# Kernel tuning notes

Measured on AMD Instinct MI355X. Metric: run time of the kernel, lower is better.

## Reference

```python
import jax, jax.numpy as jnp
import numpy as np

B, T, C, E, H = 4, 2048, 1024, 8, 4096

def setup_inputs() -> dict:
    key = jax.random.key(0)
    ks = jax.random.split(key, 5)
    x = jax.random.normal(ks[0], (B, T, C), dtype=jnp.float32)
    weights = jax.random.uniform(ks[1], (B, T, 2), dtype=jnp.float32)
    gamma = jnp.ones((C,), dtype=jnp.float32)
    beta = jnp.zeros((C,), dtype=jnp.float32)
    W1 = jax.random.normal(ks[2], (E, C, H), dtype=jnp.float32) * 0.02
    W2 = jax.random.normal(ks[3], (E, H, C), dtype=jnp.float32) * 0.02
    winners = jax.random.randint(ks[4], (B, T, 2), 0, E, dtype=jnp.int32)
    return {"x": x, "weights": weights, "gamma": gamma, "beta": beta,
            "W1": W1, "W2": W2, "winners": winners}

def _layernorm(x, gamma, beta, eps=1e-5):
    mu = jnp.mean(x, axis=-1, keepdims=True)
    var = jnp.var(x, axis=-1, keepdims=True)
    return (x - mu) * jax.lax.rsqrt(var + eps) * gamma + beta

def reference(x, weights, gamma, beta, W1, W2, winners):
    # h = ln2(x); then top-2 MoE dispatch/combine as in CaMoE_Block
    h = _layernorm(x, gamma, beta)          # [B,T,C]
    n_experts = W1.shape[0]
    final_out = jnp.zeros_like(h)
    for e in range(n_experts):
        # per-token combine coefficient: sum over the 2 ranks where winner==e
        coef = jnp.sum(jnp.where(winners == e, weights, 0.0), axis=-1)  # [B,T]
        # RWKV channel-mix FFN: relu(h W1)^2 W2
        hidden = jnp.square(jax.nn.relu(jnp.einsum('btc,ch->bth', h, W1[e])))
        expert_out = jnp.einsum('bth,hc->btc', hidden, W2[e])
        final_out = final_out + coef[..., None] * expert_out
    return x + final_out
```

## Files before the change

### kernel.cpp

```cpp
#include <hip/hip_runtime.h>
#include <stddef.h>

typedef unsigned short u16;
typedef unsigned int u32;

#define B_ 4
#define T_ 2048
#define C_ 1024
#define E_ 8
#define H_ 4096
#define NTOK (B_ * T_)
#define NPAIR (NTOK * 2)
#define BM 128
#define BN 128
#define BK 64
#define KSPLIT 2
#define MAXTILES 136
#define MAXROWS (MAXTILES * 128)
#define NWG1 ((H_ / BN) * MAXTILES)

#define NB_C2 2048
#define NB_CP 1024

#define NB_C1 2048
#define NB_LN NTOK
#define NB_CNT (NPAIR / 256)
#define NB_TID (MAXROWS / 1024)
#define NB_TOTAL (NB_C1 + NB_LN + NB_CNT + NB_TID)

typedef __bf16 bf16x8 __attribute__((ext_vector_type(8)));
typedef float f32x4 __attribute__((ext_vector_type(4)));
typedef u16 u16x8 __attribute__((ext_vector_type(8)));

__device__ __forceinline__ u16 f2bf(float f) {
    union { float f; u32 u; } c;
    c.f = f;
    u32 r = c.u + 0x7FFFu + ((c.u >> 16) & 1u);
    return (u16)(r >> 16);
}

__device__ __forceinline__ u32 pk2bf(float a, float b) {
    union { __bf16 h; u16 u; } x, y;
    x.h = (__bf16)a;
    y.h = (__bf16)b;
    return (u32)x.u | ((u32)y.u << 16);
}

__device__ __forceinline__ void gld16(const void* g, void* l) {
    __builtin_amdgcn_global_load_lds(
        (const __attribute__((address_space(1))) u32*)g,
        (__attribute__((address_space(3))) u32*)l, 16, 0, 0);
}


__device__ __forceinline__ void ln_body(
    const float* __restrict__ x, const float* __restrict__ gamma,
    const float* __restrict__ beta, u16* __restrict__ h, int token,
    float* smf) {
    const int t = threadIdx.x;
    const float* xr = x + (size_t)token * C_;
    float4 v = *(const float4*)(xr + t * 4);
    float s = v.x + v.y + v.z + v.w;
    float ss = v.x * v.x + v.y * v.y + v.z * v.z + v.w * v.w;
    #pragma unroll
    for (int off = 32; off > 0; off >>= 1) {
        s += __shfl_down(s, off);
        ss += __shfl_down(ss, off);
    }
    float* ws_s = smf;
    float* ws_q = smf + 4;
    const int wave = t >> 6, lane = t & 63;
    if (lane == 0) { ws_s[wave] = s; ws_q[wave] = ss; }
    __syncthreads();
    float S = ws_s[0] + ws_s[1] + ws_s[2] + ws_s[3];
    float Q = ws_q[0] + ws_q[1] + ws_q[2] + ws_q[3];
    float mu = S * (1.0f / C_);
    float var = Q * (1.0f / C_) - mu * mu;
    float rstd = rsqrtf(var + 1e-5f);
    float4 g = *(const float4*)(gamma + t * 4);
    float4 b = *(const float4*)(beta + t * 4);
    ushort4 hv;
    hv.x = f2bf((v.x - mu) * rstd * g.x + b.x);
    hv.y = f2bf((v.y - mu) * rstd * g.y + b.y);
    hv.z = f2bf((v.z - mu) * rstd * g.z + b.z);
    hv.w = f2bf((v.w - mu) * rstd * g.w + b.w);
    *(ushort4*)(h + (size_t)token * C_ + t * 4) = hv;
}

template <bool PERM>
__device__ __forceinline__ void conv_body(
    const float* __restrict__ in, u16* __restrict__ outp, int K, int N,
    int bid, u16* sm) {
    const int nbx = N >> 8;
    const int nby = K >> 6;
    const int bx = bid % nbx;
    const int by = (bid / nbx) % nby;
    const int e = bid / (nbx * nby);
    const int k0 = by * 64, n0 = bx * 256;
    const int t = threadIdx.x;
    const float* src = in + (size_t)e * K * N;
    u16* dst = outp + (size_t)e * N * K;
    const int cw = t & 63;
    const int rw = t >> 6;
    #pragma unroll
    for (int p = 0; p < 16; ++p) {
        const int r = p * 4 + rw;
        const int kr = PERM ? (((r & 3) << 4) | (r >> 2)) : r;
        float4 v = *(const float4*)(src + (size_t)(k0 + kr) * N + n0 + cw * 4);
        const int base = r * 258 + cw * 4;
        *(u32*)&sm[base + 0] = pk2bf(v.x, v.y);
        *(u32*)&sm[base + 2] = pk2bf(v.z, v.w);
    }
    __syncthreads();
    const u32* smw = (const u32*)sm;
    const int c = t & 7;
    const int ro = t >> 3;
    #pragma unroll
    for (int p = 0; p < 4; ++p) {
        const int np = p * 32 + ro;
        u16x8 lo, hi;
        #pragma unroll
        for (int m = 0; m < 8; ++m) {
            u32 wv = smw[(c * 8 + m) * 129 + np];
            lo[m] = (u16)(wv & 0xFFFFu);
            hi[m] = (u16)(wv >> 16);
        }
        *(u16x8*)(dst + (size_t)(n0 + 2 * np) * K + k0 + c * 8) = lo;
        *(u16x8*)(dst + (size_t)(n0 + 2 * np + 1) * K + k0 + c * 8) = hi;
    }
}

__device__ __forceinline__ void count_body(
    const int* __restrict__ winners, int* __restrict__ counts, int b, int* lc) {
    if (threadIdx.x < E_) lc[threadIdx.x] = 0;
    __syncthreads();
    atomicAdd(&lc[winners[b * 256 + threadIdx.x]], 1);
    __syncthreads();
    if (threadIdx.x < E_) {
        int c = lc[threadIdx.x];
        if (c) atomicAdd(&counts[threadIdx.x], c);
    }
}

__device__ __forceinline__ void copy_body(
    const float* __restrict__ x, float* __restrict__ out, int b) {
    const int t = threadIdx.x;
    const float4* src = (const float4*)x + (size_t)b * 2048;
    float4* dst = (float4*)out + (size_t)b * 2048;
    #pragma unroll
    for (int i = 0; i < 8; ++i) dst[i * 256 + t] = src[i * 256 + t];
}

__global__ __launch_bounds__(256) void fused_pre(
    const float* __restrict__ x, const float* __restrict__ gamma,
    const float* __restrict__ beta, u16* __restrict__ h,
    const int* __restrict__ winners, int* __restrict__ counts,
    const float* __restrict__ W1, u16* __restrict__ W1T,
    int* __restrict__ token_id) {
    __shared__ u16 sm[64 * 258];
    int b = blockIdx.x;
    if (b < NB_C1) { conv_body<false>(W1, W1T, C_, H_, b, sm); return; }
    b -= NB_C1;
    if (b < NB_LN) { ln_body(x, gamma, beta, h, b, (float*)sm); return; }
    b -= NB_LN;
    if (b < NB_CNT) { count_body(winners, counts, b, (int*)sm); return; }
    b -= NB_CNT;
    const int p = (b * 256 + threadIdx.x) * 4;
    if (p < MAXROWS) *(int4*)(token_id + p) = make_int4(-1, -1, -1, -1);
}

__global__ __launch_bounds__(256) void place_kernel(
    const int* __restrict__ winners, const float* __restrict__ wts,
    const int* __restrict__ counts, int* __restrict__ pos,
    int* __restrict__ token_id, float* __restrict__ pair_w,
    int* __restrict__ tile_expert) {
    __shared__ int po[E_ + 1];
    __shared__ int lcount[E_], lbase[E_];
    const int t = threadIdx.x;
    if (t < E_) lcount[t] = 0;
    if (t == 0) {
        int off = 0;
        po[0] = 0;
        #pragma unroll
        for (int e = 0; e < E_; ++e) {
            off += ((counts[e] + 127) >> 7) << 7;
            po[e + 1] = off;
        }
    }
    __syncthreads();
    if (blockIdx.x == 0 && t < MAXTILES) {
        int r = t * 128;
        int ee = -1;
        if (r < po[E_]) {
            ee = 0;
            while (r >= po[ee + 1]) ++ee;
        }
        tile_expert[t] = ee;
    }
    const int p = blockIdx.x * 256 + t;
    const int e = winners[p];
    const int rank = atomicAdd(&lcount[e], 1);
    __syncthreads();
    if (t < E_) {
        int c = lcount[t];
        lbase[t] = c ? atomicAdd(&pos[t], c) : 0;
    }
    __syncthreads();
    const int slot = po[e] + lbase[e] + rank;
    token_id[slot] = p >> 1;
    pair_w[slot] = wts[p];
}

template <bool PHASE2>
__device__ __forceinline__ void gemm_body(
    const u16* __restrict__ Amat, const u16* __restrict__ Bmat,
    const int* __restrict__ token_id, const float* __restrict__ pair_w,
    const int* __restrict__ tile_expert, u16* __restrict__ hidden,
    float* __restrict__ out, const u16* __restrict__ zeropage,
    int bid0, int zi, u16* __restrict__ As, u16* __restrict__ Bs) {
    constexpr int Kdim = PHASE2 ? H_ : C_;
    constexpr int KRANGE = PHASE2 ? (H_ / KSPLIT) : C_;
    constexpr int NWGX = PHASE2 ? (C_ / BN) : (H_ / BN);
    constexpr int NWG = NWGX * MAXTILES;

    int bid = (bid0 & 7) * (NWG >> 3) + (bid0 >> 3);
    const int ct = bid % NWGX;
    const int rt = bid / NWGX;

    const int e = tile_expert[rt];
    if (e < 0) return;
    const int tid = threadIdx.x;
    const int w = tid >> 6;
    const int lane = tid & 63;
    const int n0 = ct * BN;
    const int kbase = PHASE2 ? zi * KRANGE : 0;
    const u16* Bb = Bmat + (size_t)e * H_ * C_;

    const int sub = lane >> 3;
    const size_t koffB = (size_t)(((lane & 7) ^ sub) * 16);

    const char* abase[4];
    bool aval[4];
    const char* bbase[4];
    u16* adst[4];
    u16* bdst[4];
    #pragma unroll
    for (int j = 0; j < 4; ++j) {
        const int lrow32 = w * 32 + j * 8 + sub;
        const int grow = rt * BM + lrow32;
        if (PHASE2) {
            aval[j] = true;
            abase[j] = (const char*)(Amat + (size_t)grow * Kdim + kbase) + koffB;
        } else {
            int tok = token_id[grow];
            aval[j] = tok >= 0;
            abase[j] = (const char*)(Amat + (size_t)(tok < 0 ? 0 : tok) * Kdim) + koffB;
        }
        bbase[j] = (const char*)(Bb + (size_t)(n0 + lrow32) * Kdim + kbase) + koffB;
        adst[j] = &As[(w * 32 + j * 8) * BK];
        bdst[j] = &Bs[(w * 32 + j * 8) * BK];
    }

    const int wr = w >> 1, wc = w & 1;
    const int lrow = lane & 15;
    const int quad = lane >> 4;
    const int rsw = lrow & 7;

    f32x4 acc[4][4] = {};

    for (int k0 = 0; k0 < KRANGE; k0 += BK) {
        __syncthreads();
        const size_t kb = (size_t)k0 * 2;
        #pragma unroll
        for (int j = 0; j < 4; ++j)
            gld16(aval[j] ? abase[j] + kb : (const char*)zeropage, adst[j]);
        #pragma unroll
        for (int j = 0; j < 4; ++j)
            gld16(bbase[j] + kb, bdst[j]);
        __syncthreads();
        #pragma unroll
        for (int kk = 0; kk < 2; ++kk) {
            bf16x8 af[4], bfv[4];
            #pragma unroll
            for (int mi = 0; mi < 4; ++mi) {
                int row = wr * 64 + mi * 16 + lrow;
                int pch = (kk * 4 + quad) ^ rsw;
                af[mi] = *(const bf16x8*)&As[row * BK + pch * 8];
            }
            #pragma unroll
            for (int ni = 0; ni < 4; ++ni) {
                int row = wc * 64 + ni * 16 + lrow;
                int pch = (kk * 4 + quad) ^ rsw;
                bfv[ni] = *(const bf16x8*)&Bs[row * BK + pch * 8];
            }
            #pragma unroll
            for (int mi = 0; mi < 4; ++mi)
                #pragma unroll
                for (int ni = 0; ni < 4; ++ni)
                    acc[mi][ni] = __builtin_amdgcn_mfma_f32_16x16x32_bf16(
                        af[mi], bfv[ni], acc[mi][ni], 0, 0, 0);
        }
    }

    if (!PHASE2) {
        #pragma unroll
        for (int mi = 0; mi < 4; ++mi) {
            int rbase = rt * BM + wr * 64 + mi * 16 + quad * 4;
            #pragma unroll
            for (int j = 0; j < 4; ++j) {
                ushort4 o;
                float v0 = fmaxf(acc[mi][0][j], 0.0f);
                float v1 = fmaxf(acc[mi][1][j], 0.0f);
                float v2 = fmaxf(acc[mi][2][j], 0.0f);
                float v3 = fmaxf(acc[mi][3][j], 0.0f);
                o.x = f2bf(v0 * v0);
                o.y = f2bf(v1 * v1);
                o.z = f2bf(v2 * v2);
                o.w = f2bf(v3 * v3);
                *(ushort4*)&hidden[(size_t)(rbase + j) * H_ + n0 + wc * 64 + lrow * 4] = o;
            }
        }
    } else {
        #pragma unroll
        for (int mi = 0; mi < 4; ++mi) {
            int rbase = rt * BM + wr * 64 + mi * 16 + quad * 4;
            #pragma unroll
            for (int j = 0; j < 4; ++j) {
                int grow = rbase + j;
                int tok = token_id[grow];
                if (tok < 0) continue;
                float pw = pair_w[grow];
                #pragma unroll
                for (int ni = 0; ni < 4; ++ni) {
                    int col = n0 + wc * 64 + ni * 16 + lrow;
                    atomicAdd(&out[(size_t)tok * C_ + col], pw * acc[mi][ni][j]);
                }
            }
        }
    }
}

__global__ __launch_bounds__(256, 4) void gemm1_conv(
    const u16* __restrict__ h, const u16* __restrict__ W1T,
    const int* __restrict__ token_id, const float* __restrict__ pair_w,
    const int* __restrict__ tile_expert, u16* __restrict__ hidden,
    const u16* __restrict__ zeropage, const float* __restrict__ W2,
    u16* __restrict__ W2T, const float* __restrict__ x,
    float* __restrict__ out) {
    __shared__ u16 smu[64 * 258];
    const int b = blockIdx.x;
    if (b < NWG1) {
        gemm_body<false>(h, W1T, token_id, pair_w, tile_expert, hidden,
                         nullptr, zeropage, b, 0, smu, smu + BM * BK);
    } else if (b < NWG1 + NB_C2) {
        conv_body<true>(W2, W2T, H_, C_, b - NWG1, smu);
    } else {
        copy_body(x, out, b - NWG1 - NB_C2);
    }
}

__global__ __launch_bounds__(256, 4) void gemm2_kernel(
    const u16* __restrict__ hidden, const u16* __restrict__ W2T,
    const int* __restrict__ token_id, const float* __restrict__ pair_w,
    const int* __restrict__ tile_expert, float* __restrict__ out,
    const u16* __restrict__ zeropage) {
    __shared__ u16 As[BM * BK];
    __shared__ u16 Bs[BN * BK];
    const int bid = blockIdx.y * (C_ / BN) + blockIdx.x;
    gemm_body<true>(hidden, W2T, token_id, pair_w, tile_expert, nullptr, out,
                    zeropage, bid, blockIdx.z, As, Bs);
}

extern "C" void kernel_launch(void* const* d_in, const int* in_sizes, int n_in,
                              void* d_out, int out_size, void* d_ws, size_t ws_size,
                              hipStream_t stream) {
    const float* x = (const float*)d_in[0];
    const float* weights = (const float*)d_in[1];
    const float* gamma = (const float*)d_in[2];
    const float* beta = (const float*)d_in[3];
    const float* W1 = (const float*)d_in[4];
    const float* W2 = (const float*)d_in[5];
    const int* winners = (const int*)d_in[6];
    float* out = (float*)d_out;

    char* ws = (char*)d_ws;
    const size_t SZ_H = (size_t)NTOK * C_ * 2;
    const size_t SZ_HID = (size_t)MAXROWS * H_ * 2;
    const size_t SZ_WT = (size_t)E_ * H_ * C_ * 2;
    const size_t OFF_HID = SZ_H;
    const size_t OFF_W1T = OFF_HID + SZ_HID;
    const size_t OFF_W2T = OFF_W1T + SZ_WT;
    const size_t OFF_META = OFF_W2T + SZ_WT;

    u16* h = (u16*)ws;
    u16* hidden = (u16*)(ws + OFF_HID);
    u16* W1T = (u16*)(ws + OFF_W1T);
    u16* W2T = (u16*)(ws + OFF_W2T);
    int* meta = (int*)(ws + OFF_META);
    int* counts = meta;
    int* pos = meta + 8;
    u16* zeropage = (u16*)(meta + 32);
    int* tile_expert = meta + 48;
    int* token_id = meta + 192;
    float* pair_w = (float*)(meta + 192 + MAXROWS);

    hipMemsetAsync(meta, 0, 192 * sizeof(int), stream);

    fused_pre<<<NB_TOTAL, 256, 0, stream>>>(x, gamma, beta, h, winners,
                                            counts, W1, W1T, token_id);
    place_kernel<<<NPAIR / 256, 256, 0, stream>>>(winners, weights, counts, pos,
                                                  token_id, pair_w, tile_expert);
    gemm1_conv<<<NWG1 + NB_C2 + NB_CP, 256, 0, stream>>>(
        h, W1T, token_id, pair_w, tile_expert, hidden, zeropage, W2, W2T, x, out);
    gemm2_kernel<<<dim3(C_ / BN, MAXTILES, KSPLIT), 256, 0, stream>>>(
        hidden, W2T, token_id, pair_w, tile_expert, out, zeropage);
}
```

Measured before the change: 696.4 us.

## Merge preprocessing and placement kernels into one persistent kernel with grid barrier

Replaces the fused_pre and place_kernel launches with a single persistent pre_kernel of 512 blocks. Blocks first do counting, token_id init and LayerNorm, then meet at a software grid barrier before placement and W1 transpose-conversion. This removes one kernel launch and its boundary, and lets the W1 conversion run after the barrier. The cost is spin-wait barrier overhead and the risk of deadlock if not all 512 blocks are co-resident.

Result: slower. 740.3 us (+6.3%).

```diff
diff --git a/kernel.cpp b/kernel.cpp
--- a/kernel.cpp
+++ b/kernel.cpp
@@ -22,11 +22,9 @@
 #define NB_C2 2048
 #define NB_CP 1024
 
+#define NBLK_PRE 512
 #define NB_C1 2048
-#define NB_LN NTOK
 #define NB_CNT (NPAIR / 256)
-#define NB_TID (MAXROWS / 1024)
-#define NB_TOTAL (NB_C1 + NB_LN + NB_CNT + NB_TID)
 
 typedef __bf16 bf16x8 __attribute__((ext_vector_type(8)));
 typedef float f32x4 __attribute__((ext_vector_type(4)));
@@ -50,6 +48,20 @@
     __builtin_amdgcn_global_load_lds(
         (const __attribute__((address_space(1))) u32*)g,
         (__attribute__((address_space(3))) u32*)l, 16, 0, 0);
+}
+
+__device__ __forceinline__ void grid_barrier(int* bar) {
+    __syncthreads();
+    if (threadIdx.x == 0) {
+        __threadfence();
+        atomicAdd(bar, 1);
+        while (__hip_atomic_load(bar, __ATOMIC_RELAXED,
+                                 __HIP_MEMORY_SCOPE_AGENT) < NBLK_PRE) {
+            __builtin_amdgcn_s_sleep(1);
+        }
+        __threadfence();
+    }
+    __syncthreads();
 }
 
 
@@ -130,18 +142,6 @@
     }
 }
 
-__device__ __forceinline__ void count_body(
-    const int* __restrict__ winners, int* __restrict__ counts, int b, int* lc) {
-    if (threadIdx.x < E_) lc[threadIdx.x] = 0;
-    __syncthreads();
-    atomicAdd(&lc[winners[b * 256 + threadIdx.x]], 1);
-    __syncthreads();
-    if (threadIdx.x < E_) {
-        int c = lc[threadIdx.x];
-        if (c) atomicAdd(&counts[threadIdx.x], c);
-    }
-}
-
 __device__ __forceinline__ void copy_body(
     const float* __restrict__ x, float* __restrict__ out, int b) {
     const int t = threadIdx.x;
@@ -151,64 +151,83 @@
     for (int i = 0; i < 8; ++i) dst[i * 256 + t] = src[i * 256 + t];
 }
 
-__global__ __launch_bounds__(256) void fused_pre(
+__global__ __launch_bounds__(256, 4) void pre_kernel(
     const float* __restrict__ x, const float* __restrict__ gamma,
     const float* __restrict__ beta, u16* __restrict__ h,
-    const int* __restrict__ winners, int* __restrict__ counts,
+    const int* __restrict__ winners, const float* __restrict__ wts,
+    int* __restrict__ counts, int* __restrict__ pos,
     const float* __restrict__ W1, u16* __restrict__ W1T,
-    int* __restrict__ token_id) {
+    int* __restrict__ token_id, float* __restrict__ pair_w,
+    int* __restrict__ tile_expert, int* __restrict__ bar) {
     __shared__ u16 sm[64 * 258];
-    int b = blockIdx.x;
-    if (b < NB_C1) { conv_body<false>(W1, W1T, C_, H_, b, sm); return; }
-    b -= NB_C1;
-    if (b < NB_LN) { ln_body(x, gamma, beta, h, b, (float*)sm); return; }
-    b -= NB_LN;
-    if (b < NB_CNT) { count_body(winners, counts, b, (int*)sm); return; }
-    b -= NB_CNT;
-    const int p = (b * 256 + threadIdx.x) * 4;
-    if (p < MAXROWS) *(int4*)(token_id + p) = make_int4(-1, -1, -1, -1);
-}
-
-__global__ __launch_bounds__(256) void place_kernel(
-    const int* __restrict__ winners, const float* __restrict__ wts,
-    const int* __restrict__ counts, int* __restrict__ pos,
-    int* __restrict__ token_id, float* __restrict__ pair_w,
-    int* __restrict__ tile_expert) {
-    __shared__ int po[E_ + 1];
-    __shared__ int lcount[E_], lbase[E_];
+    int* smi = (int*)sm;
+    const int b = blockIdx.x;
     const int t = threadIdx.x;
-    if (t < E_) lcount[t] = 0;
-    if (t == 0) {
-        int off = 0;
-        po[0] = 0;
-        #pragma unroll
-        for (int e = 0; e < E_; ++e) {
-            off += ((counts[e] + 127) >> 7) << 7;
-            po[e + 1] = off;
-        }
-    }
-    __syncthreads();
-    if (blockIdx.x == 0 && t < MAXTILES) {
-        int r = t * 128;
-        int ee = -1;
-        if (r < po[E_]) {
-            ee = 0;
-            while (r >= po[ee + 1]) ++ee;
-        }
-        tile_expert[t] = ee;
-    }
-    const int p = blockIdx.x * 256 + t;
-    const int e = winners[p];
-    const int rank = atomicAdd(&lcount[e], 1);
-    __syncthreads();
-    if (t < E_) {
-        int c = lcount[t];
-        lbase[t] = c ? atomicAdd(&pos[t], c) : 0;
-    }
-    __syncthreads();
-    const int slot = po[e] + lbase[e] + rank;
-    token_id[slot] = p >> 1;
-    pair_w[slot] = wts[p];
+
+    {
+        const int idx = b * 256 + t;
+        if (idx < MAXROWS) token_id[idx] = -1;
+    }
+    if (b < NB_CNT) {
+        int* lc = smi;
+        if (t < E_) lc[t] = 0;
+        __syncthreads();
+        atomicAdd(&lc[winners[b * 256 + t]], 1);
+        __syncthreads();
+        if (t < E_) {
+            int c = lc[t];
+            if (c) atomicAdd(&counts[t], c);
+        }
+    }
+    for (int tok = b; tok < NTOK; tok += NBLK_PRE) {
+        ln_body(x, gamma, beta, h, tok, (float*)(smi + 16));
+        __syncthreads();
+    }
+
+    grid_barrier(bar);
+
+    if (b < NB_CNT) {
+        int* po = smi;
+        int* lcount = smi + 12;
+        int* lbase = smi + 20;
+        if (t < E_) lcount[t] = 0;
+        if (t == 0) {
+            int off = 0;
+            po[0] = 0;
+            #pragma unroll
+            for (int e = 0; e < E_; ++e) {
+                off += ((counts[e] + 127) >> 7) << 7;
+                po[e + 1] = off;
+            }
+        }
+        __syncthreads();
+        if (b == 0 && t < MAXTILES) {
+            int r = t * 128;
+            int ee = -1;
+            if (r < po[E_]) {
+                ee = 0;
+                while (r >= po[ee + 1]) ++ee;
+            }
+            tile_expert[t] = ee;
+        }
+        const int p = b * 256 + t;
+        const int e = winners[p];
+        const int rank = atomicAdd(&lcount[e], 1);
+        __syncthreads();
+        if (t < E_) {
+            int c = lcount[t];
+            lbase[t] = c ? atomicAdd(&pos[t], c) : 0;
+        }
+        __syncthreads();
+        const int slot = po[e] + lbase[e] + rank;
+        token_id[slot] = p >> 1;
+        pair_w[slot] = wts[p];
+        __syncthreads();
+    }
+    for (int tile = b; tile < NB_C1; tile += NBLK_PRE) {
+        conv_body<false>(W1, W1T, C_, H_, tile, sm);
+        __syncthreads();
+    }
 }
 
 template <bool PHASE2>
@@ -399,6 +418,7 @@
     int* meta = (int*)(ws + OFF_META);
     int* counts = meta;
     int* pos = meta + 8;
+    int* bar = meta + 16;
     u16* zeropage = (u16*)(meta + 32);
     int* tile_expert = meta + 48;
     int* token_id = meta + 192;
@@ -406,10 +426,9 @@
 
     hipMemsetAsync(meta, 0, 192 * sizeof(int), stream);
 
-    fused_pre<<<NB_TOTAL, 256, 0, stream>>>(x, gamma, beta, h, winners,
-                                            counts, W1, W1T, token_id);
-    place_kernel<<<NPAIR / 256, 256, 0, stream>>>(winners, weights, counts, pos,
-                                                  token_id, pair_w, tile_expert);
+    pre_kernel<<<NBLK_PRE, 256, 0, stream>>>(
+        x, gamma, beta, h, winners, weights, counts, pos, W1, W1T,
+        token_id, pair_w, tile_expert, bar);
     gemm1_conv<<<NWG1 + NB_C2 + NB_CP, 256, 0, stream>>>(
         h, W1T, token_id, pair_w, tile_expert, hidden, zeropage, W2, W2T, x, out);
     gemm2_kernel<<<dim3(C_ / BN, MAXTILES, KSPLIT), 256, 0, stream>>>(
```
